# Kernel tuning notes

Hardware: AMD Instinct MI355X
Metric: run time of the kernel (lower is better)

The kernel has to match this reference:

```python
import jax, jax.numpy as jnp
import numpy as np

B, SEED, GEN = 32, 128, 384
IN, H, OUT = 171, 1024, 171


def setup_inputs() -> dict:
    key = jax.random.key(0)
    ks = jax.random.split(key, 16)
    s = 0.05
    w = lambda k, shape: (jax.random.normal(k, shape, jnp.float32) * s)
    inp = {
        "seed_seq": jax.random.normal(ks[0], (B, SEED, IN), jnp.float32),
        "Wih1": w(ks[1], (4 * H, IN)),  "Whh1": w(ks[2], (4 * H, H)),
        "bih1": w(ks[3], (4 * H,)),     "bhh1": w(ks[4], (4 * H,)),
        "Wih2": w(ks[5], (4 * H, H)),   "Whh2": w(ks[6], (4 * H, H)),
        "bih2": w(ks[7], (4 * H,)),     "bhh2": w(ks[8], (4 * H,)),
        "Wih3": w(ks[9], (4 * H, H)),   "Whh3": w(ks[10], (4 * H, H)),
        "bih3": w(ks[11], (4 * H,)),    "bhh3": w(ks[12], (4 * H,)),
        "Wdec": w(ks[13], (OUT, H)),    "bdec": w(ks[14], (OUT,)),
        "gen_len": GEN,
    }
    return inp


def _lstm_cell(x, h, c, Wih, Whh, bih, bhh):
    # PyTorch LSTMCell: gate order i, f, g, o
    gates = x @ Wih.T + bih + h @ Whh.T + bhh  # [B, 4H]
    i, f, g, o = jnp.split(gates, 4, axis=-1)
    c_new = jax.nn.sigmoid(f) * c + jax.nn.sigmoid(i) * jnp.tanh(g)
    h_new = jax.nn.sigmoid(o) * jnp.tanh(c_new)
    return h_new, c_new


def reference(seed_seq, Wih1, Whh1, bih1, bhh1, Wih2, Whh2, bih2, bhh2,
              Wih3, Whh3, bih3, bhh3, Wdec, bdec, gen_len):
    batch = seed_seq.shape[0]
    hsz = Whh1.shape[1]
    z = jnp.zeros((batch, hsz), seed_seq.dtype)

    def step(state, x):
        h1, c1, h2, c2, h3, c3 = state
        h1, c1 = _lstm_cell(x, h1, c1, Wih1, Whh1, bih1, bhh1)
        h2, c2 = _lstm_cell(h1, h2, c2, Wih2, Whh2, bih2, bhh2)
        h3, c3 = _lstm_cell(h2, h3, c3, Wih3, Whh3, bih3, bhh3)
        out = h3 @ Wdec.T + bdec
        return (h1, c1, h2, c2, h3, c3), out

    # conditioning (seed) phase: scan over time-major seed sequence
    state0 = (z, z, z, z, z, z)
    state, seed_outs = jax.lax.scan(step, state0, jnp.swapaxes(seed_seq, 0, 1))

    def gen_step(carry, _):
        cur, st = carry
        st, out = step(st, cur)
        return (out, st), out

    _, gen_outs = jax.lax.scan(gen_step, (seed_outs[-1], state), None, length=gen_len)

    outs = jnp.concatenate([seed_outs, gen_outs], axis=0)  # [T, B, OUT]
    return jnp.swapaxes(outs, 0, 1)  # [B, T, OUT]
```

## Files before the change

kernel.cpp:

```cpp
#include <hip/hip_runtime.h>
#include <hip/hip_bf16.h>
#include <math.h>

#define NB    32
#define NSEED 128
#define NTT   512
#define NIN   171
#define NINP  192
#define NH    1024
#define NG    4096
#define NOUT  171
#define NOUTP 176
#define NWG   256

typedef unsigned short u16;
typedef unsigned int u32;
typedef __attribute__((ext_vector_type(8))) short bf16x8;
typedef __attribute__((ext_vector_type(4))) float f32x4;
typedef __attribute__((ext_vector_type(4))) int i32x4;

__device__ __host__ inline u16 f2bf(float x) {
  union { float f; unsigned u; } v; v.f = x;
  unsigned r = v.u + 0x7FFFu + ((v.u >> 16) & 1u);
  return (u16)(r >> 16);
}

__global__ void pack_mat(const float* __restrict__ src, u16* __restrict__ dst, int ktiles) {
  int id = blockIdx.x * 256 + threadIdx.x;
  int total = ktiles * 256 * 64;
  if (id >= total) return;
  int lane = id & 63;
  int nt = (id >> 6) & 255;
  int kt = id >> 14;
  int c = lane & 15, q = lane >> 4;
  int r = (c & 3) * 1024 + nt * 4 + (c >> 2);
  int K = ktiles * 32;
  const float* s = src + (size_t)r * K + kt * 32 + q * 8;
  __attribute__((aligned(16))) u16 o[8];
#pragma unroll
  for (int j = 0; j < 8; ++j) o[j] = f2bf(s[j]);
  *(bf16x8*)(dst + (size_t)id * 8) = *(const bf16x8*)o;
}

__global__ void pack_wih1(const float* __restrict__ src, u16* __restrict__ dst) {
  int id = blockIdx.x * 256 + threadIdx.x;
  if (id >= 6 * 256 * 64) return;
  int lane = id & 63;
  int nt = (id >> 6) & 255;
  int kt = id >> 14;
  int c = lane & 15, q = lane >> 4;
  int r = (c & 3) * 1024 + nt * 4 + (c >> 2);
  int k0 = kt * 32 + q * 8;
  __attribute__((aligned(16))) u16 o[8];
#pragma unroll
  for (int j = 0; j < 8; ++j) {
    int k = k0 + j;
    o[j] = (k < NIN) ? f2bf(src[(size_t)r * NIN + k]) : (u16)0;
  }
  *(bf16x8*)(dst + (size_t)id * 8) = *(const bf16x8*)o;
}

__global__ void pack_wdec(const float* __restrict__ src, u16* __restrict__ dst) {
  int id = blockIdx.x * 256 + threadIdx.x;
  if (id >= 32 * 11 * 64) return;
  int lane = id & 63;
  int nt = (id >> 6) % 11;
  int kt = (id >> 6) / 11;
  int c = lane & 15, q = lane >> 4;
  int r = nt * 16 + c;
  int k0 = kt * 32 + q * 8;
  __attribute__((aligned(16))) u16 o[8];
#pragma unroll
  for (int j = 0; j < 8; ++j) {
    o[j] = (r < NOUT) ? f2bf(src[(size_t)r * NH + k0 + j]) : (u16)0;
  }
  *(bf16x8*)(dst + (size_t)id * 8) = *(const bf16x8*)o;
}

__global__ void pack_seed(const float* __restrict__ src, u16* __restrict__ dst) {
  int id = blockIdx.x * 256 + threadIdx.x;
  if (id >= NSEED * NB * NINP) return;
  int kp = id % NINP;
  int b = (id / NINP) % NB;
  int t = id / (NINP * NB);
  float v = (kp < NIN) ? src[((size_t)b * NSEED + t) * NIN + kp] : 0.f;
  dst[id] = f2bf(v);
}

__global__ void wfuse_kernel(const float* __restrict__ wih1, const float* __restrict__ wdec,
                             float* __restrict__ tmp) {
  int n = blockIdx.x;
  int k = blockIdx.y * 256 + threadIdx.x;
  const float* wr = wih1 + (size_t)n * NIN;
  float s = 0.f;
  for (int i = 0; i < NIN; ++i) s += wr[i] * wdec[(size_t)i * NH + k];
  tmp[(size_t)n * NH + k] = s;
}

__global__ void prep_bias(const float* bih1, const float* bhh1, const float* bih2, const float* bhh2,
                          const float* bih3, const float* bhh3, const float* __restrict__ wih1,
                          const float* __restrict__ bdec_in,
                          float* b1s, float* b1g, float* b2, float* b3, float* bdecp,
                          int* __restrict__ flags) {
  int n = blockIdx.x * 256 + threadIdx.x;
  if (n >= NG) return;
  int wgi = n >> 4, c = n & 15;
  int r = (c & 3) * 1024 + wgi * 4 + (c >> 2);
  float v1 = bih1[r] + bhh1[r];
  b1s[n] = v1;
  float bf = 0.f;
  for (int i = 0; i < NIN; ++i) bf += wih1[(size_t)r * NIN + i] * bdec_in[i];
  b1g[n] = v1 + bf;
  b2[n] = bih2[r] + bhh2[r];
  b3[n] = bih3[r] + bhh3[r];
  if (n < NOUTP) bdecp[n] = (n < NOUT) ? bdec_in[n] : 0.f;
  if (n < NWG) flags[n] = 0;
}

__device__ __forceinline__ float fsig(float x) {
  return __builtin_amdgcn_rcpf(1.f + __expf(-x));
}
__device__ __forceinline__ float ftanh(float x) {
  return 1.f - 2.f * __builtin_amdgcn_rcpf(1.f + __expf(2.f * x));
}

#define MFMA_BF16 __builtin_amdgcn_mfma_f32_16x16x32_bf16

__device__ __forceinline__ void mm32_lds(f32x4& d0, f32x4& d1, const u16* wl,
                                         const u16* __restrict__ x, int wv, int lane) {
  int m = lane & 15, q = lane >> 4;
  const u16* xa = x + m * NH + q * 8 + wv * 32;
  const u16* xb = xa + 16 * NH;
  const u16* wb = wl + lane * 8;
  bf16x8 w[8], a0[8], a1[8];
#pragma unroll
  for (int i = 0; i < 8; ++i) {
    a0[i] = *(const bf16x8*)(xa + i * 128);
    a1[i] = *(const bf16x8*)(xb + i * 128);
  }
#pragma unroll
  for (int i = 0; i < 8; ++i) w[i] = *(const bf16x8*)(wb + (size_t)(wv + 4 * i) * 512);
#pragma unroll
  for (int i = 0; i < 8; ++i) {
    d0 = MFMA_BF16(a0[i], w[i], d0, 0, 0, 0);
    d1 = MFMA_BF16(a1[i], w[i], d1, 0, 0, 0);
  }
}

__device__ __forceinline__ void mm32_glb(f32x4& d0, f32x4& d1, const u16* __restrict__ wgb,
                                         const u16* __restrict__ x, int wv, int lane) {
  int m = lane & 15, q = lane >> 4;
  const u16* xa = x + m * NH + q * 8 + wv * 32;
  const u16* xb = xa + 16 * NH;
  const u16* wb = wgb + lane * 8;
  bf16x8 w[8], a0[8], a1[8];
#pragma unroll
  for (int i = 0; i < 8; ++i) {
    a0[i] = *(const bf16x8*)(xa + i * 128);
    a1[i] = *(const bf16x8*)(xb + i * 128);
  }
#pragma unroll
  for (int i = 0; i < 8; ++i) w[i] = *(const bf16x8*)(wb + (size_t)(wv + 4 * i) * 131072);
#pragma unroll
  for (int i = 0; i < 8; ++i) {
    d0 = MFMA_BF16(a0[i], w[i], d0, 0, 0, 0);
    d1 = MFMA_BF16(a1[i], w[i], d1, 0, 0, 0);
  }
}

__device__ __forceinline__ void mm6_glb(f32x4& d0, f32x4& d1, const u16* __restrict__ wbase,
                                        const u16* __restrict__ x, int wv, int lane) {
  int m = lane & 15, q = lane >> 4;
  const u16* xa = x + m * NINP + q * 8;
  const u16* xb = xa + 16 * NINP;
  const u16* wb = wbase + lane * 8;
#pragma unroll
  for (int i = 0; i < 2; ++i) {
    int kt = wv + 4 * i;
    if (kt >= 6) break;
    bf16x8 w = *(const bf16x8*)(wb + (size_t)kt * 131072);
    bf16x8 a0 = *(const bf16x8*)(xa + kt * 32);
    bf16x8 a1 = *(const bf16x8*)(xb + kt * 32);
    d0 = MFMA_BF16(a0, w, d0, 0, 0, 0);
    d1 = MFMA_BF16(a1, w, d1, 0, 0, 0);
  }
}

__global__ __launch_bounds__(256, 1) void lstm_main(
    const u16* __restrict__ whh1, const u16* __restrict__ whh2, const u16* __restrict__ whh3,
    const u16* __restrict__ wih2, const u16* __restrict__ wih3,
    const u16* __restrict__ wfuse, const u16* __restrict__ wih1,
    const u16* __restrict__ seedp,
    u16* __restrict__ h1h, u16* __restrict__ h2h, u16* __restrict__ h3h,
    const float* __restrict__ b1s, const float* __restrict__ b1g,
    const float* __restrict__ b2, const float* __restrict__ b3,
    int* __restrict__ flags)
{
  __shared__ u16  wlds[4 * 16384];
  __shared__ float red[4][64][8];
  __shared__ float biasLds[4][16];
  __shared__ float cst[3][32][4];

  int wg = blockIdx.x;
  int tid = threadIdx.x;
  int wv = tid >> 6, lane = tid & 63;

  {
    const u16* srcs[4] = { wih2 + (size_t)wg * 512, wih3 + (size_t)wg * 512,
                           wfuse + (size_t)wg * 512, whh1 + (size_t)wg * 512 };
#pragma unroll
    for (int m = 0; m < 4; ++m) {
      for (int i = tid; i < 2048; i += 256) {
        int kt = i >> 6, ln = i & 63;
        *(bf16x8*)&wlds[m * 16384 + (kt * 64 + ln) * 8] =
            *(const bf16x8*)(srcs[m] + ((size_t)kt * 16384 + ln) * 8);
      }
    }
    float* cp = &cst[0][0][0];
    for (int i = tid; i < 3 * 32 * 4; i += 256) cp[i] = 0.f;
    if (tid < 64) {
      int row = tid >> 4, c = tid & 15;
      const float* src = (row == 0) ? b1s : (row == 1) ? b1g : (row == 2) ? b2 : b3;
      biasLds[row][c] = src[wg * 16 + c];
    }
  }
  __syncthreads();

  const u16* whh2g = whh2 + (size_t)wg * 512;
  const u16* whh3g = whh3 + (size_t)wg * 512;
  const u16* wih1g = wih1 + (size_t)wg * 512;

  int ep = 0;
  for (int t = 0; t < NTT; ++t) {
    for (int l = 0; l < 3; ++l) {
      f32x4 d0 = {0.f, 0.f, 0.f, 0.f}, d1 = {0.f, 0.f, 0.f, 0.f};
      bool isseed = (t < NSEED);

      if (l == 0 && isseed)
        mm6_glb(d0, d1, wih1g, seedp + (size_t)t * NB * NINP, wv, lane);
      if (t > 0) {
        if (l == 0)
          mm32_lds(d0, d1, &wlds[3 * 16384], h1h + (size_t)(t - 1) * NB * NH, wv, lane);
        else if (l == 1)
          mm32_glb(d0, d1, whh2g, h2h + (size_t)(t - 1) * NB * NH, wv, lane);
        else
          mm32_glb(d0, d1, whh3g, h3h + (size_t)(t - 1) * NB * NH, wv, lane);
      }

      bool skipwait = (l == 0 && isseed);
      if (ep > 0 && !skipwait && wv == 1) {
        const int* fp = flags + (lane << 2);
        for (;;) {
          i32x4 f;
          asm volatile("global_load_dwordx4 %0, %1, off sc0 sc1\n\ts_waitcnt vmcnt(0)"
                       : "=v"(f) : "v"(fp) : "memory");
          int mn = min(min(f.x, f.y), min(f.z, f.w));
          if (__all(mn >= ep)) break;
          __builtin_amdgcn_s_sleep(1);
        }
      }
      __syncthreads();

      if (l == 0) {
        if (!isseed)
          mm32_lds(d0, d1, &wlds[2 * 16384], h3h + (size_t)(t - 1) * NB * NH, wv, lane);
      } else {
        const u16* xs = (l == 1) ? h1h + (size_t)t * NB * NH
                                 : h2h + (size_t)t * NB * NH;
        mm32_lds(d0, d1, &wlds[(l - 1) * 16384], xs, wv, lane);
      }

#pragma unroll
      for (int r = 0; r < 4; ++r) { red[wv][lane][r] = d0[r]; red[wv][lane][4 + r] = d1[r]; }
      __syncthreads();

      int epn = ep + 1;
      if (tid < 64) {
        __builtin_amdgcn_s_setprio(1);
        int b = tid & 31, upair = tid >> 5;
        int srcl_base = ((b & 15) >> 2) << 4;
        int idx = ((b >> 4) << 2) | (b & 3);
        int bsel = (l == 0) ? (isseed ? 0 : 1) : (l + 1);
        float g[8];
#pragma unroll
        for (int u2 = 0; u2 < 2; ++u2) {
          int u = upair * 2 + u2;
#pragma unroll
          for (int gi = 0; gi < 4; ++gi) {
            int c = u * 4 + gi;
            int srcl = srcl_base | c;
            g[u2 * 4 + gi] = red[0][srcl][idx] + red[1][srcl][idx] +
                             red[2][srcl][idx] + red[3][srcl][idx] + biasLds[bsel][c];
          }
        }
        unsigned hv[2];
#pragma unroll
        for (int u2 = 0; u2 < 2; ++u2) {
          int u = upair * 2 + u2;
          float si = fsig(g[u2 * 4 + 0]);
          float sf = fsig(g[u2 * 4 + 1]);
          float so = fsig(g[u2 * 4 + 3]);
          float cn = sf * cst[l][b][u] + si * ftanh(g[u2 * 4 + 2]);
          cst[l][b][u] = cn;
          hv[u2] = (unsigned)f2bf(so * ftanh(cn));
        }
        unsigned val = hv[0] | (hv[1] << 16);
        u16* hdst = (l == 0) ? h1h + (size_t)t * NB * NH
                  : (l == 1) ? h2h + (size_t)t * NB * NH
                             : h3h + (size_t)t * NB * NH;
        u32* hp = (u32*)hdst + (size_t)b * 512 + wg * 2 + upair;
        __hip_atomic_store(hp, val, __ATOMIC_RELAXED, __HIP_MEMORY_SCOPE_AGENT);
        asm volatile("s_waitcnt vmcnt(0)" ::: "memory");
        if (tid == 0)
          __hip_atomic_store(&flags[wg], epn, __ATOMIC_RELAXED, __HIP_MEMORY_SCOPE_AGENT);
        __builtin_amdgcn_s_setprio(0);
      }
      ep = epn;
    }
  }
}

__global__ __launch_bounds__(256) void dec_kernel(
    const u16* __restrict__ h3h, const u16* __restrict__ wdec,
    const float* __restrict__ bdecp, float* __restrict__ out)
{
  int task = blockIdx.x * 4 + (threadIdx.x >> 6);
  int lane = threadIdx.x & 63;
  int nt = task % 11, rt = task / 11;
  if (rt >= NTT) return;
  int m = lane & 15, q = lane >> 4;
  const u16* xa = h3h + ((size_t)rt * 32 + m) * NH + q * 8;
  const u16* xb = xa + (size_t)16 * NH;
  f32x4 d0 = {0.f, 0.f, 0.f, 0.f}, d1 = {0.f, 0.f, 0.f, 0.f};
  for (int kt = 0; kt < 32; ++kt) {
    bf16x8 bf = *(const bf16x8*)(wdec + ((size_t)(kt * 11 + nt) * 64 + lane) * 8);
    bf16x8 a0 = *(const bf16x8*)(xa + kt * 32);
    bf16x8 a1 = *(const bf16x8*)(xb + kt * 32);
    d0 = MFMA_BF16(a0, bf, d0, 0, 0, 0);
    d1 = MFMA_BF16(a1, bf, d1, 0, 0, 0);
  }
  int o = nt * 16 + m;
  if (o >= NOUT) return;
  float bv = bdecp[o];
#pragma unroll
  for (int reg = 0; reg < 4; ++reg) {
    int row0 = rt * 32 + q * 4 + reg;
    out[(((size_t)(row0 & 31)) * NTT + (row0 >> 5)) * NOUT + o] = d0[reg] + bv;
    int row1 = row0 + 16;
    out[(((size_t)(row1 & 31)) * NTT + (row1 >> 5)) * NOUT + o] = d1[reg] + bv;
  }
}

extern "C" void kernel_launch(void* const* d_in, const int* in_sizes, int n_in,
                              void* d_out, int out_size, void* d_ws, size_t ws_size,
                              hipStream_t stream) {
  const float* seed = (const float*)d_in[0];
  const float* Wih1 = (const float*)d_in[1];
  const float* Whh1 = (const float*)d_in[2];
  const float* bih1 = (const float*)d_in[3];
  const float* bhh1 = (const float*)d_in[4];
  const float* Wih2 = (const float*)d_in[5];
  const float* Whh2 = (const float*)d_in[6];
  const float* bih2 = (const float*)d_in[7];
  const float* bhh2 = (const float*)d_in[8];
  const float* Wih3 = (const float*)d_in[9];
  const float* Whh3 = (const float*)d_in[10];
  const float* bih3 = (const float*)d_in[11];
  const float* bhh3 = (const float*)d_in[12];
  const float* Wdec = (const float*)d_in[13];
  const float* bdec = (const float*)d_in[14];

  char* ws = (char*)d_ws;
  size_t off = 0;
  auto alloc = [&](size_t bytes) -> void* {
    void* p = ws + off;
    off += (bytes + 63) & ~(size_t)63;
    return p;
  };
  const size_t BIGPK = (size_t)32 * 256 * 64 * 8 * 2;
  const size_t HHIST = (size_t)NTT * NB * NH * 2;
  u16* whh1p  = (u16*)alloc(BIGPK);
  u16* whh2p  = (u16*)alloc(BIGPK);
  u16* whh3p  = (u16*)alloc(BIGPK);
  u16* wih2p  = (u16*)alloc(BIGPK);
  u16* wih3p  = (u16*)alloc(BIGPK);
  u16* wfusep = (u16*)alloc(BIGPK);
  u16* wih1p  = (u16*)alloc((size_t)6 * 256 * 64 * 8 * 2);
  u16* wdecp  = (u16*)alloc((size_t)32 * 11 * 64 * 8 * 2);
  u16* seedp  = (u16*)alloc((size_t)NSEED * NB * NINP * 2);
  u16* h1h    = (u16*)alloc(HHIST);
  u16* h2h    = (u16*)alloc(HHIST);
  u16* h3h    = (u16*)alloc(HHIST);
  float* b1s  = (float*)alloc((size_t)NG * 4);
  float* b1g  = (float*)alloc((size_t)NG * 4);
  float* b2   = (float*)alloc((size_t)NG * 4);
  float* b3   = (float*)alloc((size_t)NG * 4);
  float* bdecp = (float*)alloc((size_t)NOUTP * 4);
  int* flags  = (int*)alloc((size_t)NWG * 4);
  float* wftmp = (float*)h3h;

  pack_mat<<<dim3(2048), dim3(256), 0, stream>>>(Whh1, whh1p, 32);
  pack_mat<<<dim3(2048), dim3(256), 0, stream>>>(Whh2, whh2p, 32);
  pack_mat<<<dim3(2048), dim3(256), 0, stream>>>(Whh3, whh3p, 32);
  pack_mat<<<dim3(2048), dim3(256), 0, stream>>>(Wih2, wih2p, 32);
  pack_mat<<<dim3(2048), dim3(256), 0, stream>>>(Wih3, wih3p, 32);
  pack_wih1<<<dim3(384), dim3(256), 0, stream>>>(Wih1, wih1p);
  wfuse_kernel<<<dim3(4096, 4), dim3(256), 0, stream>>>(Wih1, Wdec, wftmp);
  pack_mat<<<dim3(2048), dim3(256), 0, stream>>>(wftmp, wfusep, 32);
  pack_wdec<<<dim3(88), dim3(256), 0, stream>>>(Wdec, wdecp);
  pack_seed<<<dim3(3072), dim3(256), 0, stream>>>(seed, seedp);
  prep_bias<<<dim3(16), dim3(256), 0, stream>>>(bih1, bhh1, bih2, bhh2, bih3, bhh3,
                                                Wih1, bdec, b1s, b1g, b2, b3, bdecp, flags);
  lstm_main<<<dim3(NWG), dim3(256), 0, stream>>>(
      whh1p, whh2p, whh3p, wih2p, wih3p, wfusep, wih1p, seedp,
      h1h, h2h, h3h, b1s, b1g, b2, b3, flags);
  dec_kernel<<<dim3(1408), dim3(256), 0, stream>>>(h3h, wdecp, bdecp, (float*)d_out);
}
```

Baseline: 6.708 ms.

## Split wave roles: three waves compute recurrent GEMM while wave 1 polls flags

Restructures the per-layer step so the recurrent (previous-timestep) matmul is spread across waves 1-3 in K-chunks while wave 0 stays idle on that part. The flag-poll load is issued first and its wait is deferred until after the precompute, overlapping the poll latency with useful work. Partial sums go into extra reduction slots in LDS, and the cell update sums them conditionally. This removes the ordering where all recurrent work finished before polling started, but it leaves load imbalance because wave 0 does no precompute and wave 1 both computes and polls.

Measured after the change: 8.160 ms. 1.22x slower.

```diff
diff --git a/kernel.cpp b/kernel.cpp
--- a/kernel.cpp
+++ b/kernel.cpp
@@ -147,37 +147,39 @@
   }
 }
 
-__device__ __forceinline__ void mm32_glb(f32x4& d0, f32x4& d1, const u16* __restrict__ wgb,
-                                         const u16* __restrict__ x, int wv, int lane) {
+__device__ __forceinline__ void mmk_pre(f32x4& d0, f32x4& d1, const u16* wbase, int wstride,
+                                        const u16* __restrict__ x, int kt0, int nchunk,
+                                        int lane) {
   int m = lane & 15, q = lane >> 4;
-  const u16* xa = x + m * NH + q * 8 + wv * 32;
+  const u16* xa = x + m * NH + q * 8;
   const u16* xb = xa + 16 * NH;
-  const u16* wb = wgb + lane * 8;
-  bf16x8 w[8], a0[8], a1[8];
-#pragma unroll
-  for (int i = 0; i < 8; ++i) {
-    a0[i] = *(const bf16x8*)(xa + i * 128);
-    a1[i] = *(const bf16x8*)(xb + i * 128);
-  }
-#pragma unroll
-  for (int i = 0; i < 8; ++i) w[i] = *(const bf16x8*)(wb + (size_t)(wv + 4 * i) * 131072);
-#pragma unroll
-  for (int i = 0; i < 8; ++i) {
-    d0 = MFMA_BF16(a0[i], w[i], d0, 0, 0, 0);
-    d1 = MFMA_BF16(a1[i], w[i], d1, 0, 0, 0);
-  }
-}
-
-__device__ __forceinline__ void mm6_glb(f32x4& d0, f32x4& d1, const u16* __restrict__ wbase,
-                                        const u16* __restrict__ x, int wv, int lane) {
+  const u16* wb = wbase + lane * 8;
+  for (int c = 0; c < nchunk; ++c) {
+    int kb = kt0 + c * 4;
+    bf16x8 a0[4], a1[4], w[4];
+#pragma unroll
+    for (int i = 0; i < 4; ++i) {
+      a0[i] = *(const bf16x8*)(xa + (kb + i) * 32);
+      a1[i] = *(const bf16x8*)(xb + (kb + i) * 32);
+      w[i]  = *(const bf16x8*)(wb + (size_t)(kb + i) * wstride);
+    }
+#pragma unroll
+    for (int i = 0; i < 4; ++i) {
+      d0 = MFMA_BF16(a0[i], w[i], d0, 0, 0, 0);
+      d1 = MFMA_BF16(a1[i], w[i], d1, 0, 0, 0);
+    }
+  }
+}
+
+__device__ __forceinline__ void mm6_pre(f32x4& d0, f32x4& d1, const u16* __restrict__ wbase,
+                                        const u16* __restrict__ x, int kt0, int lane) {
   int m = lane & 15, q = lane >> 4;
   const u16* xa = x + m * NINP + q * 8;
   const u16* xb = xa + 16 * NINP;
   const u16* wb = wbase + lane * 8;
 #pragma unroll
   for (int i = 0; i < 2; ++i) {
-    int kt = wv + 4 * i;
-    if (kt >= 6) break;
+    int kt = kt0 + 3 * i;
     bf16x8 w = *(const bf16x8*)(wb + (size_t)kt * 131072);
     bf16x8 a0 = *(const bf16x8*)(xa + kt * 32);
     bf16x8 a1 = *(const bf16x8*)(xb + kt * 32);
@@ -197,7 +199,7 @@
     int* __restrict__ flags)
 {
   __shared__ u16  wlds[4 * 16384];
-  __shared__ float red[4][64][8];
+  __shared__ float red[7][64][8];
   __shared__ float biasLds[4][16];
   __shared__ float cst[3][32][4];
 
@@ -229,49 +231,65 @@
   const u16* whh2g = whh2 + (size_t)wg * 512;
   const u16* whh3g = whh3 + (size_t)wg * 512;
   const u16* wih1g = wih1 + (size_t)wg * 512;
+  const int* fp = flags + (lane << 2);
 
   int ep = 0;
   for (int t = 0; t < NTT; ++t) {
     for (int l = 0; l < 3; ++l) {
-      f32x4 d0 = {0.f, 0.f, 0.f, 0.f}, d1 = {0.f, 0.f, 0.f, 0.f};
       bool isseed = (t < NSEED);
-
-      if (l == 0 && isseed)
-        mm6_glb(d0, d1, wih1g, seedp + (size_t)t * NB * NINP, wv, lane);
-      if (t > 0) {
-        if (l == 0)
-          mm32_lds(d0, d1, &wlds[3 * 16384], h1h + (size_t)(t - 1) * NB * NH, wv, lane);
-        else if (l == 1)
-          mm32_glb(d0, d1, whh2g, h2h + (size_t)(t - 1) * NB * NH, wv, lane);
-        else
-          mm32_glb(d0, d1, whh3g, h3h + (size_t)(t - 1) * NB * NH, wv, lane);
-      }
-
       bool skipwait = (l == 0 && isseed);
-      if (ep > 0 && !skipwait && wv == 1) {
-        const int* fp = flags + (lane << 2);
+      bool dowait = (ep > 0 && !skipwait);
+      bool haspre = (t > 0) || skipwait;
+      bool hasfresh = !skipwait;
+
+      i32x4 fpoll;
+      if (dowait && wv == 1)
+        asm volatile("global_load_dwordx4 %0, %1, off sc0 sc1" : "=v"(fpoll) : "v"(fp));
+
+      f32x4 dp0 = {0.f, 0.f, 0.f, 0.f}, dp1 = {0.f, 0.f, 0.f, 0.f};
+      if (wv != 0 && haspre) {
+        int wvm1 = wv - 1;
+        int kt0 = wvm1 * 12;
+        int nch = (wvm1 == 2) ? 2 : 3;
+        if (l == 0) {
+          if (isseed)
+            mm6_pre(dp0, dp1, wih1g, seedp + (size_t)t * NB * NINP, wvm1, lane);
+          if (t > 0)
+            mmk_pre(dp0, dp1, &wlds[3 * 16384], 512,
+                    h1h + (size_t)(t - 1) * NB * NH, kt0, nch, lane);
+        } else if (l == 1) {
+          mmk_pre(dp0, dp1, whh2g, 131072, h2h + (size_t)(t - 1) * NB * NH, kt0, nch, lane);
+        } else {
+          mmk_pre(dp0, dp1, whh3g, 131072, h3h + (size_t)(t - 1) * NB * NH, kt0, nch, lane);
+        }
+      }
+
+      if (dowait && wv == 1) {
+        asm volatile("s_waitcnt vmcnt(0)" ::: "memory");
         for (;;) {
-          i32x4 f;
-          asm volatile("global_load_dwordx4 %0, %1, off sc0 sc1\n\ts_waitcnt vmcnt(0)"
-                       : "=v"(f) : "v"(fp) : "memory");
-          int mn = min(min(f.x, f.y), min(f.z, f.w));
+          int mn = min(min(fpoll.x, fpoll.y), min(fpoll.z, fpoll.w));
           if (__all(mn >= ep)) break;
           __builtin_amdgcn_s_sleep(1);
+          asm volatile("global_load_dwordx4 %0, %1, off sc0 sc1\n\ts_waitcnt vmcnt(0)"
+                       : "=v"(fpoll) : "v"(fp) : "memory");
         }
       }
       __syncthreads();
 
-      if (l == 0) {
-        if (!isseed)
+      if (wv != 0 && haspre) {
+#pragma unroll
+        for (int r = 0; r < 4; ++r) { red[3 + wv][lane][r] = dp0[r]; red[3 + wv][lane][4 + r] = dp1[r]; }
+      }
+      if (hasfresh) {
+        f32x4 d0 = {0.f, 0.f, 0.f, 0.f}, d1 = {0.f, 0.f, 0.f, 0.f};
+        if (l == 0)
           mm32_lds(d0, d1, &wlds[2 * 16384], h3h + (size_t)(t - 1) * NB * NH, wv, lane);
-      } else {
-        const u16* xs = (l == 1) ? h1h + (size_t)t * NB * NH
-                                 : h2h + (size_t)t * NB * NH;
-        mm32_lds(d0, d1, &wlds[(l - 1) * 16384], xs, wv, lane);
-      }
-
-#pragma unroll
-      for (int r = 0; r < 4; ++r) { red[wv][lane][r] = d0[r]; red[wv][lane][4 + r] = d1[r]; }
+        else
+          mm32_lds(d0, d1, &wlds[(l - 1) * 16384],
+                   ((l == 1) ? h1h : h2h) + (size_t)t * NB * NH, wv, lane);
+#pragma unroll
+        for (int r = 0; r < 4; ++r) { red[wv][lane][r] = d0[r]; red[wv][lane][4 + r] = d1[r]; }
+      }
       __syncthreads();
 
       int epn = ep + 1;
@@ -284,13 +302,17 @@
         float g[8];
 #pragma unroll
         for (int u2 = 0; u2 < 2; ++u2) {
-          int u = upair * 2 + u2;
 #pragma unroll
           for (int gi = 0; gi < 4; ++gi) {
-            int c = u * 4 + gi;
+            int c = (upair * 2 + u2) * 4 + gi;
             int srcl = srcl_base | c;
-            g[u2 * 4 + gi] = red[0][srcl][idx] + red[1][srcl][idx] +
-                             red[2][srcl][idx] + red[3][srcl][idx] + biasLds[bsel][c];
+            float s = biasLds[bsel][c];
+            if (hasfresh)
+              s += red[0][srcl][idx] + red[1][srcl][idx] +
+                   red[2][srcl][idx] + red[3][srcl][idx];
+            if (haspre)
+              s += red[4][srcl][idx] + red[5][srcl][idx] + red[6][srcl][idx];
+            g[u2 * 4 + gi] = s;
           }
         }
         unsigned hv[2];
```

## Keep fetched hidden-state fragments in registers for reuse across LSTM layers

Applied to the files above, without the earlier changes.

The per-timestep layer loop is unrolled into three explicit blocks. Each hidden-state activation fragment loaded after a barrier (h1, h2, h3) is kept in registers and reused as the operand of the matching recurrent or input GEMM in the next layer step or timestep. This removes a second global load of the same h vectors per step. The cost is much higher register pressure (48 bf16x8 vectors held live), which with one workgroup per CU may cause spills, plus duplicated code.

Result: slower. 9.688 ms (+44.4%).

```diff
diff --git a/kernel.cpp b/kernel.cpp
--- a/kernel.cpp
+++ b/kernel.cpp
@@ -124,26 +124,57 @@
   return 1.f - 2.f * __builtin_amdgcn_rcpf(1.f + __expf(2.f * x));
 }
 
+#define MFMA_BF16 __builtin_amdgcn_mfma_f32_16x32_bf16_ERR
+#undef MFMA_BF16
 #define MFMA_BF16 __builtin_amdgcn_mfma_f32_16x16x32_bf16
 
-__device__ __forceinline__ void mm32_lds(f32x4& d0, f32x4& d1, const u16* wl,
-                                         const u16* __restrict__ x, int wv, int lane) {
+__device__ __forceinline__ void mm32_fresh(f32x4& d0, f32x4& d1, const u16* wl,
+                                           const u16* __restrict__ x, int wv, int lane,
+                                           bf16x8 (&sa0)[8], bf16x8 (&sa1)[8]) {
   int m = lane & 15, q = lane >> 4;
   const u16* xa = x + m * NH + q * 8 + wv * 32;
   const u16* xb = xa + 16 * NH;
   const u16* wb = wl + lane * 8;
-  bf16x8 w[8], a0[8], a1[8];
+  bf16x8 w[8];
 #pragma unroll
   for (int i = 0; i < 8; ++i) {
-    a0[i] = *(const bf16x8*)(xa + i * 128);
-    a1[i] = *(const bf16x8*)(xb + i * 128);
+    sa0[i] = *(const bf16x8*)(xa + i * 128);
+    sa1[i] = *(const bf16x8*)(xb + i * 128);
   }
 #pragma unroll
   for (int i = 0; i < 8; ++i) w[i] = *(const bf16x8*)(wb + (size_t)(wv + 4 * i) * 512);
 #pragma unroll
   for (int i = 0; i < 8; ++i) {
-    d0 = MFMA_BF16(a0[i], w[i], d0, 0, 0, 0);
-    d1 = MFMA_BF16(a1[i], w[i], d1, 0, 0, 0);
+    d0 = MFMA_BF16(sa0[i], w[i], d0, 0, 0, 0);
+    d1 = MFMA_BF16(sa1[i], w[i], d1, 0, 0, 0);
+  }
+}
+
+__device__ __forceinline__ void mm32_pre_lds(f32x4& d0, f32x4& d1, const u16* wl,
+                                             int wv, int lane,
+                                             const bf16x8 (&sa0)[8], const bf16x8 (&sa1)[8]) {
+  const u16* wb = wl + lane * 8;
+  bf16x8 w[8];
+#pragma unroll
+  for (int i = 0; i < 8; ++i) w[i] = *(const bf16x8*)(wb + (size_t)(wv + 4 * i) * 512);
+#pragma unroll
+  for (int i = 0; i < 8; ++i) {
+    d0 = MFMA_BF16(sa0[i], w[i], d0, 0, 0, 0);
+    d1 = MFMA_BF16(sa1[i], w[i], d1, 0, 0, 0);
+  }
+}
+
+__device__ __forceinline__ void mm32_pre_glb(f32x4& d0, f32x4& d1, const u16* __restrict__ wgb,
+                                             int wv, int lane,
+                                             const bf16x8 (&sa0)[8], const bf16x8 (&sa1)[8]) {
+  const u16* wb = wgb + lane * 8;
+  bf16x8 w[8];
+#pragma unroll
+  for (int i = 0; i < 8; ++i) w[i] = *(const bf16x8*)(wb + (size_t)(wv + 4 * i) * 131072);
+#pragma unroll
+  for (int i = 0; i < 8; ++i) {
+    d0 = MFMA_BF16(sa0[i], w[i], d0, 0, 0, 0);
+    d1 = MFMA_BF16(sa1[i], w[i], d1, 0, 0, 0);
   }
 }
 
@@ -183,6 +214,18 @@
     bf16x8 a1 = *(const bf16x8*)(xb + kt * 32);
     d0 = MFMA_BF16(a0, w, d0, 0, 0, 0);
     d1 = MFMA_BF16(a1, w, d1, 0, 0, 0);
+  }
+}
+
+__device__ __forceinline__ void pollwait(const int* __restrict__ flags, int lane, int ep) {
+  const int* fp = flags + (lane << 2);
+  for (;;) {
+    i32x4 f;
+    asm volatile("global_load_dwordx4 %0, %1, off sc0 sc1\n\ts_waitcnt vmcnt(0)"
+                 : "=v"(f) : "v"(fp) : "memory");
+    int mn = min(min(f.x, f.y), min(f.z, f.w));
+    if (__all(mn >= ep)) break;
+    __builtin_amdgcn_s_sleep(1);
   }
 }
 
@@ -230,69 +273,43 @@
   const u16* whh3g = whh3 + (size_t)wg * 512;
   const u16* wih1g = wih1 + (size_t)wg * 512;
 
+  bf16x8 s0a[8], s0b[8], s1a[8], s1b[8], s2a[8], s2b[8];
+
   int ep = 0;
   for (int t = 0; t < NTT; ++t) {
-    for (int l = 0; l < 3; ++l) {
+    bool isseed = (t < NSEED);
+
+    {
       f32x4 d0 = {0.f, 0.f, 0.f, 0.f}, d1 = {0.f, 0.f, 0.f, 0.f};
-      bool isseed = (t < NSEED);
-
-      if (l == 0 && isseed)
+      if (isseed)
         mm6_glb(d0, d1, wih1g, seedp + (size_t)t * NB * NINP, wv, lane);
-      if (t > 0) {
-        if (l == 0)
-          mm32_lds(d0, d1, &wlds[3 * 16384], h1h + (size_t)(t - 1) * NB * NH, wv, lane);
-        else if (l == 1)
-          mm32_glb(d0, d1, whh2g, h2h + (size_t)(t - 1) * NB * NH, wv, lane);
-        else
-          mm32_glb(d0, d1, whh3g, h3h + (size_t)(t - 1) * NB * NH, wv, lane);
-      }
-
-      bool skipwait = (l == 0 && isseed);
-      if (ep > 0 && !skipwait && wv == 1) {
-        const int* fp = flags + (lane << 2);
-        for (;;) {
-          i32x4 f;
-          asm volatile("global_load_dwordx4 %0, %1, off sc0 sc1\n\ts_waitcnt vmcnt(0)"
-                       : "=v"(f) : "v"(fp) : "memory");
-          int mn = min(min(f.x, f.y), min(f.z, f.w));
-          if (__all(mn >= ep)) break;
-          __builtin_amdgcn_s_sleep(1);
-        }
-      }
+      if (t > 0)
+        mm32_pre_lds(d0, d1, &wlds[3 * 16384], wv, lane, s1a, s1b);
+      if (ep > 0 && !isseed && wv == 1) pollwait(flags, lane, ep);
       __syncthreads();
-
-      if (l == 0) {
-        if (!isseed)
-          mm32_lds(d0, d1, &wlds[2 * 16384], h3h + (size_t)(t - 1) * NB * NH, wv, lane);
-      } else {
-        const u16* xs = (l == 1) ? h1h + (size_t)t * NB * NH
-                                 : h2h + (size_t)t * NB * NH;
-        mm32_lds(d0, d1, &wlds[(l - 1) * 16384], xs, wv, lane);
-      }
-
+      if (!isseed)
+        mm32_fresh(d0, d1, &wlds[2 * 16384], h3h + (size_t)(t - 1) * NB * NH,
+                   wv, lane, s0a, s0b);
 #pragma unroll
       for (int r = 0; r < 4; ++r) { red[wv][lane][r] = d0[r]; red[wv][lane][4 + r] = d1[r]; }
       __syncthreads();
-
       int epn = ep + 1;
       if (tid < 64) {
         __builtin_amdgcn_s_setprio(1);
         int b = tid & 31, upair = tid >> 5;
         int srcl_base = ((b & 15) >> 2) << 4;
         int idx = ((b >> 4) << 2) | (b & 3);
-        int bsel = (l == 0) ? (isseed ? 0 : 1) : (l + 1);
+        int bsel = isseed ? 0 : 1;
         float g[8];
 #pragma unroll
-        for (int u2 = 0; u2 < 2; ++u2) {
-          int u = upair * 2 + u2;
+        for (int u2 = 0; u2 < 2; ++u2)
 #pragma unroll
           for (int gi = 0; gi < 4; ++gi) {
-            int c = u * 4 + gi;
+            int c = (upair * 2 + u2) * 4 + gi;
             int srcl = srcl_base | c;
             g[u2 * 4 + gi] = red[0][srcl][idx] + red[1][srcl][idx] +
                              red[2][srcl][idx] + red[3][srcl][idx] + biasLds[bsel][c];
           }
-        }
         unsigned hv[2];
 #pragma unroll
         for (int u2 = 0; u2 < 2; ++u2) {
@@ -300,15 +317,112 @@
           float si = fsig(g[u2 * 4 + 0]);
           float sf = fsig(g[u2 * 4 + 1]);
           float so = fsig(g[u2 * 4 + 3]);
-          float cn = sf * cst[l][b][u] + si * ftanh(g[u2 * 4 + 2]);
-          cst[l][b][u] = cn;
+          float cn = sf * cst[0][b][u] + si * ftanh(g[u2 * 4 + 2]);
+          cst[0][b][u] = cn;
           hv[u2] = (unsigned)f2bf(so * ftanh(cn));
         }
         unsigned val = hv[0] | (hv[1] << 16);
-        u16* hdst = (l == 0) ? h1h + (size_t)t * NB * NH
-                  : (l == 1) ? h2h + (size_t)t * NB * NH
-                             : h3h + (size_t)t * NB * NH;
-        u32* hp = (u32*)hdst + (size_t)b * 512 + wg * 2 + upair;
+        u32* hp = (u32*)(h1h + (size_t)t * NB * NH) + (size_t)b * 512 + wg * 2 + upair;
+        __hip_atomic_store(hp, val, __ATOMIC_RELAXED, __HIP_MEMORY_SCOPE_AGENT);
+        asm volatile("s_waitcnt vmcnt(0)" ::: "memory");
+        if (tid == 0)
+          __hip_atomic_store(&flags[wg], epn, __ATOMIC_RELAXED, __HIP_MEMORY_SCOPE_AGENT);
+        __builtin_amdgcn_s_setprio(0);
+      }
+      ep = epn;
+    }
+
+    {
+      f32x4 d0 = {0.f, 0.f, 0.f, 0.f}, d1 = {0.f, 0.f, 0.f, 0.f};
+      if (t > 0)
+        mm32_pre_glb(d0, d1, whh2g, wv, lane, s2a, s2b);
+      if (wv == 1) pollwait(flags, lane, ep);
+      __syncthreads();
+      mm32_fresh(d0, d1, &wlds[0], h1h + (size_t)t * NB * NH, wv, lane, s1a, s1b);
+#pragma unroll
+      for (int r = 0; r < 4; ++r) { red[wv][lane][r] = d0[r]; red[wv][lane][4 + r] = d1[r]; }
+      __syncthreads();
+      int epn = ep + 1;
+      if (tid < 64) {
+        __builtin_amdgcn_s_setprio(1);
+        int b = tid & 31, upair = tid >> 5;
+        int srcl_base = ((b & 15) >> 2) << 4;
+        int idx = ((b >> 4) << 2) | (b & 3);
+        float g[8];
+#pragma unroll
+        for (int u2 = 0; u2 < 2; ++u2)
+#pragma unroll
+          for (int gi = 0; gi < 4; ++gi) {
+            int c = (upair * 2 + u2) * 4 + gi;
+            int srcl = srcl_base | c;
+            g[u2 * 4 + gi] = red[0][srcl][idx] + red[1][srcl][idx] +
+                             red[2][srcl][idx] + red[3][srcl][idx] + biasLds[2][c];
+          }
+        unsigned hv[2];
+#pragma unroll
+        for (int u2 = 0; u2 < 2; ++u2) {
+          int u = upair * 2 + u2;
+          float si = fsig(g[u2 * 4 + 0]);
+          float sf = fsig(g[u2 * 4 + 1]);
+          float so = fsig(g[u2 * 4 + 3]);
+          float cn = sf * cst[1][b][u] + si * ftanh(g[u2 * 4 + 2]);
+          cst[1][b][u] = cn;
+          hv[u2] = (unsigned)f2bf(so * ftanh(cn));
+        }
+        unsigned val = hv[0] | (hv[1] << 16);
+        u32* hp = (u32*)(h2h + (size_t)t * NB * NH) + (size_t)b * 512 + wg * 2 + upair;
+        __hip_atomic_store(hp, val, __ATOMIC_RELAXED, __HIP_MEMORY_SCOPE_AGENT);
+        asm volatile("s_waitcnt vmcnt(0)" ::: "memory");
+        if (tid == 0)
+          __hip_atomic_store(&flags[wg], epn, __ATOMIC_RELAXED, __HIP_MEMORY_SCOPE_AGENT);
+        __builtin_amdgcn_s_setprio(0);
+      }
+      ep = epn;
+    }
+
+    {
+      f32x4 d0 = {0.f, 0.f, 0.f, 0.f}, d1 = {0.f, 0.f, 0.f, 0.f};
+      if (t > 0) {
+        if (isseed)
+          mm32_glb(d0, d1, whh3g, h3h + (size_t)(t - 1) * NB * NH, wv, lane);
+        else
+          mm32_pre_glb(d0, d1, whh3g, wv, lane, s0a, s0b);
+      }
+      if (wv == 1) pollwait(flags, lane, ep);
+      __syncthreads();
+      mm32_fresh(d0, d1, &wlds[1 * 16384], h2h + (size_t)t * NB * NH, wv, lane, s2a, s2b);
+#pragma unroll
+      for (int r = 0; r < 4; ++r) { red[wv][lane][r] = d0[r]; red[wv][lane][4 + r] = d1[r]; }
+      __syncthreads();
+      int epn = ep + 1;
+      if (tid < 64) {
+        __builtin_amdgcn_s_setprio(1);
+        int b = tid & 31, upair = tid >> 5;
+        int srcl_base = ((b & 15) >> 2) << 4;
+        int idx = ((b >> 4) << 2) | (b & 3);
+        float g[8];
+#pragma unroll
+        for (int u2 = 0; u2 < 2; ++u2)
+#pragma unroll
+          for (int gi = 0; gi < 4; ++gi) {
+            int c = (upair * 2 + u2) * 4 + gi;
+            int srcl = srcl_base | c;
+            g[u2 * 4 + gi] = red[0][srcl][idx] + red[1][srcl][idx] +
+                             red[2][srcl][idx] + red[3][srcl][idx] + biasLds[3][c];
+          }
+        unsigned hv[2];
+#pragma unroll
+        for (int u2 = 0; u2 < 2; ++u2) {
+          int u = upair * 2 + u2;
+          float si = fsig(g[u2 * 4 + 0]);
+          float sf = fsig(g[u2 * 4 + 1]);
+          float so = fsig(g[u2 * 4 + 3]);
+          float cn = sf * cst[2][b][u] + si * ftanh(g[u2 * 4 + 2]);
+          cst[2][b][u] = cn;
+          hv[u2] = (unsigned)f2bf(so * ftanh(cn));
+        }
+        unsigned val = hv[0] | (hv[1] << 16);
+        u32* hp = (u32*)(h3h + (size_t)t * NB * NH) + (size_t)b * 512 + wg * 2 + upair;
         __hip_atomic_store(hp, val, __ATOMIC_RELAXED, __HIP_MEMORY_SCOPE_AGENT);
         asm volatile("s_waitcnt vmcnt(0)" ::: "memory");
         if (tid == 0)
```

## Split matmul K across waves 1-3, reserve wave 0 for gates, prefetch fresh inputs before barrier

Applied to the files above, without the earlier changes.

Each layer step's K dimension is now split across waves 1-3 instead of all four waves, which frees wave 0 to do only the gate/reduction work. Waves 1-3 each poll the flags themselves, then load the freshly produced hidden-state activations into registers before the barrier. After the barrier only the LDS-weight MFMAs remain on the critical path. The intent is to shorten the latency between a flag being seen and the matmul finishing. In exchange, each compute wave does more MFMA work and uses more registers, and only three waves share the matmul.

Measured after the change: 8.042 ms. 19.9% more time.

```diff
diff --git a/kernel.cpp b/kernel.cpp
--- a/kernel.cpp
+++ b/kernel.cpp
@@ -126,63 +126,79 @@
 
 #define MFMA_BF16 __builtin_amdgcn_mfma_f32_16x16x32_bf16
 
-__device__ __forceinline__ void mm32_lds(f32x4& d0, f32x4& d1, const u16* wl,
-                                         const u16* __restrict__ x, int wv, int lane) {
+template<int K0, int K1>
+__device__ __forceinline__ void pre_mm_h(f32x4& d0, f32x4& d1, const u16* wbase, size_t wstride,
+                                         const u16* __restrict__ x, int lane) {
   int m = lane & 15, q = lane >> 4;
-  const u16* xa = x + m * NH + q * 8 + wv * 32;
+  const u16* xa = x + m * NH + q * 8;
   const u16* xb = xa + 16 * NH;
-  const u16* wb = wl + lane * 8;
-  bf16x8 w[8], a0[8], a1[8];
-#pragma unroll
-  for (int i = 0; i < 8; ++i) {
-    a0[i] = *(const bf16x8*)(xa + i * 128);
-    a1[i] = *(const bf16x8*)(xb + i * 128);
-  }
-#pragma unroll
-  for (int i = 0; i < 8; ++i) w[i] = *(const bf16x8*)(wb + (size_t)(wv + 4 * i) * 512);
-#pragma unroll
-  for (int i = 0; i < 8; ++i) {
+  const u16* wb = wbase + lane * 8;
+  bf16x8 a0[K1 - K0], a1[K1 - K0], w[K1 - K0];
+#pragma unroll
+  for (int i = 0; i < K1 - K0; ++i) {
+    a0[i] = *(const bf16x8*)(xa + (K0 + i) * 32);
+    a1[i] = *(const bf16x8*)(xb + (K0 + i) * 32);
+  }
+#pragma unroll
+  for (int i = 0; i < K1 - K0; ++i) w[i] = *(const bf16x8*)(wb + (size_t)(K0 + i) * wstride);
+#pragma unroll
+  for (int i = 0; i < K1 - K0; ++i) {
     d0 = MFMA_BF16(a0[i], w[i], d0, 0, 0, 0);
     d1 = MFMA_BF16(a1[i], w[i], d1, 0, 0, 0);
   }
 }
 
-__device__ __forceinline__ void mm32_glb(f32x4& d0, f32x4& d1, const u16* __restrict__ wgb,
-                                         const u16* __restrict__ x, int wv, int lane) {
-  int m = lane & 15, q = lane >> 4;
-  const u16* xa = x + m * NH + q * 8 + wv * 32;
-  const u16* xb = xa + 16 * NH;
-  const u16* wb = wgb + lane * 8;
-  bf16x8 w[8], a0[8], a1[8];
-#pragma unroll
-  for (int i = 0; i < 8; ++i) {
-    a0[i] = *(const bf16x8*)(xa + i * 128);
-    a1[i] = *(const bf16x8*)(xb + i * 128);
-  }
-#pragma unroll
-  for (int i = 0; i < 8; ++i) w[i] = *(const bf16x8*)(wb + (size_t)(wv + 4 * i) * 131072);
-#pragma unroll
-  for (int i = 0; i < 8; ++i) {
-    d0 = MFMA_BF16(a0[i], w[i], d0, 0, 0, 0);
-    d1 = MFMA_BF16(a1[i], w[i], d1, 0, 0, 0);
-  }
-}
-
-__device__ __forceinline__ void mm6_glb(f32x4& d0, f32x4& d1, const u16* __restrict__ wbase,
-                                        const u16* __restrict__ x, int wv, int lane) {
+template<int K0, int K1>
+__device__ __forceinline__ void pre_mm6(f32x4& d0, f32x4& d1, const u16* __restrict__ wbase,
+                                        const u16* __restrict__ x, int lane) {
   int m = lane & 15, q = lane >> 4;
   const u16* xa = x + m * NINP + q * 8;
   const u16* xb = xa + 16 * NINP;
   const u16* wb = wbase + lane * 8;
 #pragma unroll
-  for (int i = 0; i < 2; ++i) {
-    int kt = wv + 4 * i;
-    if (kt >= 6) break;
-    bf16x8 w = *(const bf16x8*)(wb + (size_t)kt * 131072);
-    bf16x8 a0 = *(const bf16x8*)(xa + kt * 32);
-    bf16x8 a1 = *(const bf16x8*)(xb + kt * 32);
+  for (int i = 0; i < K1 - K0; ++i) {
+    bf16x8 w = *(const bf16x8*)(wb + (size_t)(K0 + i) * 131072);
+    bf16x8 a0 = *(const bf16x8*)(xa + (K0 + i) * 32);
+    bf16x8 a1 = *(const bf16x8*)(xb + (K0 + i) * 32);
     d0 = MFMA_BF16(a0, w, d0, 0, 0, 0);
     d1 = MFMA_BF16(a1, w, d1, 0, 0, 0);
+  }
+}
+
+template<int K0, int K1>
+__device__ __forceinline__ void fresh_ld(const u16* __restrict__ x, int lane,
+                                         bf16x8* a0, bf16x8* a1) {
+  int m = lane & 15, q = lane >> 4;
+  const u16* xa = x + m * NH + q * 8;
+  const u16* xb = xa + 16 * NH;
+#pragma unroll
+  for (int i = 0; i < K1 - K0; ++i) {
+    a0[i] = *(const bf16x8*)(xa + (K0 + i) * 32);
+    a1[i] = *(const bf16x8*)(xb + (K0 + i) * 32);
+  }
+}
+
+template<int K0, int K1>
+__device__ __forceinline__ void fresh_mm(f32x4& d0, f32x4& d1, const u16* wl, int lane,
+                                         const bf16x8* a0, const bf16x8* a1) {
+  const u16* wb = wl + lane * 8;
+#pragma unroll
+  for (int i = 0; i < K1 - K0; ++i) {
+    bf16x8 w = *(const bf16x8*)(wb + (size_t)(K0 + i) * 512);
+    d0 = MFMA_BF16(a0[i], w, d0, 0, 0, 0);
+    d1 = MFMA_BF16(a1[i], w, d1, 0, 0, 0);
+  }
+}
+
+__device__ __forceinline__ void pollwait(const int* __restrict__ flags, int lane, int ep) {
+  const int* fp = flags + (lane << 2);
+  for (;;) {
+    i32x4 f;
+    asm volatile("global_load_dwordx4 %0, %1, off sc0 sc1\n\ts_waitcnt vmcnt(0)"
+                 : "=v"(f) : "v"(fp) : "memory");
+    int mn = min(min(f.x, f.y), min(f.z, f.w));
+    if (__all(mn >= ep)) break;
+    __builtin_amdgcn_s_sleep(1);
   }
 }
 
@@ -233,45 +249,58 @@
   int ep = 0;
   for (int t = 0; t < NTT; ++t) {
     for (int l = 0; l < 3; ++l) {
+      bool isseed = (t < NSEED);
+      bool skipwait = (l == 0 && isseed);
+      bool dowait = (ep > 0 && !skipwait);
+      bool hasfresh = !skipwait;
+      bool haspre = (t > 0) || skipwait;
+
       f32x4 d0 = {0.f, 0.f, 0.f, 0.f}, d1 = {0.f, 0.f, 0.f, 0.f};
-      bool isseed = (t < NSEED);
-
-      if (l == 0 && isseed)
-        mm6_glb(d0, d1, wih1g, seedp + (size_t)t * NB * NINP, wv, lane);
-      if (t > 0) {
-        if (l == 0)
-          mm32_lds(d0, d1, &wlds[3 * 16384], h1h + (size_t)(t - 1) * NB * NH, wv, lane);
-        else if (l == 1)
-          mm32_glb(d0, d1, whh2g, h2h + (size_t)(t - 1) * NB * NH, wv, lane);
-        else
-          mm32_glb(d0, d1, whh3g, h3h + (size_t)(t - 1) * NB * NH, wv, lane);
-      }
-
-      bool skipwait = (l == 0 && isseed);
-      if (ep > 0 && !skipwait && wv == 1) {
-        const int* fp = flags + (lane << 2);
-        for (;;) {
-          i32x4 f;
-          asm volatile("global_load_dwordx4 %0, %1, off sc0 sc1\n\ts_waitcnt vmcnt(0)"
-                       : "=v"(f) : "v"(fp) : "memory");
-          int mn = min(min(f.x, f.y), min(f.z, f.w));
-          if (__all(mn >= ep)) break;
-          __builtin_amdgcn_s_sleep(1);
+      bf16x8 fa0[11], fa1[11];
+
+      if (wv != 0) {
+        if (haspre) {
+          const u16* xpre; const u16* wpre; size_t wps;
+          if (l == 0)      { xpre = h1h + (size_t)(t - 1) * NB * NH; wpre = &wlds[3 * 16384]; wps = 512; }
+          else if (l == 1) { xpre = h2h + (size_t)(t - 1) * NB * NH; wpre = whh2g; wps = 131072; }
+          else             { xpre = h3h + (size_t)(t - 1) * NB * NH; wpre = whh3g; wps = 131072; }
+          if (l == 0 && isseed) {
+            const u16* xs = seedp + (size_t)t * NB * NINP;
+            if (wv == 1)      pre_mm6<0, 2>(d0, d1, wih1g, xs, lane);
+            else if (wv == 2) pre_mm6<2, 4>(d0, d1, wih1g, xs, lane);
+            else              pre_mm6<4, 6>(d0, d1, wih1g, xs, lane);
+          }
+          if (t > 0) {
+            if (wv == 1)      pre_mm_h<0, 10>(d0, d1, wpre, wps, xpre, lane);
+            else if (wv == 2) pre_mm_h<10, 21>(d0, d1, wpre, wps, xpre, lane);
+            else              pre_mm_h<21, 32>(d0, d1, wpre, wps, xpre, lane);
+          }
+        }
+        if (dowait) pollwait(flags, lane, ep);
+        if (hasfresh) {
+          const u16* xfr = (l == 0) ? h3h + (size_t)(t - 1) * NB * NH
+                         : (l == 1) ? h1h + (size_t)t * NB * NH
+                                    : h2h + (size_t)t * NB * NH;
+          if (wv == 1)      fresh_ld<0, 11>(xfr, lane, fa0, fa1);
+          else if (wv == 2) fresh_ld<11, 22>(xfr, lane, fa0, fa1);
+          else              fresh_ld<22, 32>(xfr, lane, fa0, fa1);
         }
       }
-      __syncthreads();
-
-      if (l == 0) {
-        if (!isseed)
-          mm32_lds(d0, d1, &wlds[2 * 16384], h3h + (size_t)(t - 1) * NB * NH, wv, lane);
-      } else {
-        const u16* xs = (l == 1) ? h1h + (size_t)t * NB * NH
-                                 : h2h + (size_t)t * NB * NH;
-        mm32_lds(d0, d1, &wlds[(l - 1) * 16384], xs, wv, lane);
+
+      asm volatile("s_barrier" ::: "memory");
+
+      if (wv != 0) {
+        if (hasfresh) {
+          const u16* wfr = (l == 0) ? &wlds[2 * 16384]
+                         : (l == 1) ? &wlds[0]
+                                    : &wlds[1 * 16384];
+          if (wv == 1)      fresh_mm<0, 11>(d0, d1, wfr, lane, fa0, fa1);
+          else if (wv == 2) fresh_mm<11, 22>(d0, d1, wfr, lane, fa0, fa1);
+          else              fresh_mm<22, 32>(d0, d1, wfr, lane, fa0, fa1);
+        }
+#pragma unroll
+        for (int r = 0; r < 4; ++r) { red[wv][lane][r] = d0[r]; red[wv][lane][4 + r] = d1[r]; }
       }
-
-#pragma unroll
-      for (int r = 0; r < 4; ++r) { red[wv][lane][r] = d0[r]; red[wv][lane][4 + r] = d1[r]; }
       __syncthreads();
 
       int epn = ep + 1;
@@ -283,16 +312,14 @@
         int bsel = (l == 0) ? (isseed ? 0 : 1) : (l + 1);
         float g[8];
 #pragma unroll
-        for (int u2 = 0; u2 < 2; ++u2) {
-          int u = upair * 2 + u2;
+        for (int u2 = 0; u2 < 2; ++u2)
 #pragma unroll
           for (int gi = 0; gi < 4; ++gi) {
-            int c = u * 4 + gi;
+            int c = (upair * 2 + u2) * 4 + gi;
             int srcl = srcl_base | c;
-            g[u2 * 4 + gi] = red[0][srcl][idx] + red[1][srcl][idx] +
-                             red[2][srcl][idx] + red[3][srcl][idx] + biasLds[bsel][c];
+            g[u2 * 4 + gi] = red[1][srcl][idx] + red[2][srcl][idx] +
+                             red[3][srcl][idx] + biasLds[bsel][c];
           }
-        }
         unsigned hv[2];
 #pragma unroll
         for (int u2 = 0; u2 < 2; ++u2) {
```
